# Performance work log

Hardware: AMD Instinct MI355X
Metric: run time of the kernel (lower is better)

Reference implementation:

```python
import jax, jax.numpy as jnp
import numpy as np

N, E, FI, H, T, FO, B = 20000, 320000, 16, 100, 5, 20, 50
EPS = 1e-5


def _glorot(k, shape, fan_in):
    return jax.random.normal(k, shape, jnp.float32) / np.float32(np.sqrt(fan_in))


def setup_inputs():
    key = jax.random.key(0)
    ks = jax.random.split(key, 16)
    inp = {}
    inp['x'] = jax.random.normal(ks[0], (N, FI), jnp.float32)
    inp['edge_index'] = jax.random.randint(ks[1], (2, E), 0, N, jnp.int32)
    inp['edge_attr'] = jax.random.normal(ks[2], (E, 1), jnp.float32)
    inp['batch'] = jnp.sort(jax.random.randint(ks[3], (N,), 0, B, jnp.int32))
    # PNAConv layer 0: input_dim -> hidden (F_in=FI, F_out=FO per tower)
    inp['e0_w'] = _glorot(ks[4], (1, FI), 1); inp['e0_b'] = jnp.zeros((FI,), jnp.float32)
    inp['pre0_w'] = _glorot(ks[5], (T, 3 * FI, FI), 3 * FI); inp['pre0_b'] = jnp.zeros((T, FI), jnp.float32)
    inp['post0_w'] = _glorot(ks[6], (T, 17 * FI, FO), 17 * FI); inp['post0_b'] = jnp.zeros((T, FO), jnp.float32)
    inp['lin0_w'] = _glorot(ks[7], (H, H), H); inp['lin0_b'] = jnp.zeros((H,), jnp.float32)
    inp['bn0_g'] = jnp.ones((H,), jnp.float32); inp['bn0_b'] = jnp.zeros((H,), jnp.float32)
    # PNAConv layers 1..2 (hidden -> hidden), stacked on leading dim 2
    inp['eL_w'] = _glorot(ks[8], (2, 1, H), 1); inp['eL_b'] = jnp.zeros((2, H), jnp.float32)
    inp['preL_w'] = _glorot(ks[9], (2, T, 3 * H, H), 3 * H); inp['preL_b'] = jnp.zeros((2, T, H), jnp.float32)
    inp['postL_w'] = _glorot(ks[10], (2, T, 17 * H, FO), 17 * H); inp['postL_b'] = jnp.zeros((2, T, FO), jnp.float32)
    inp['linL_w'] = _glorot(ks[11], (2, H, H), H); inp['linL_b'] = jnp.zeros((2, H), jnp.float32)
    inp['bnL_g'] = jnp.ones((2, H), jnp.float32); inp['bnL_b'] = jnp.zeros((2, H), jnp.float32)
    # head MLP: H -> 50 -> 25 -> 1
    inp['mlp_w1'] = _glorot(ks[12], (H, 50), H); inp['mlp_b1'] = jnp.zeros((50,), jnp.float32)
    inp['mlp_w2'] = _glorot(ks[13], (50, 25), 50); inp['mlp_b2'] = jnp.zeros((25,), jnp.float32)
    inp['mlp_w3'] = _glorot(ks[14], (25, 1), 25); inp['mlp_b3'] = jnp.zeros((1,), jnp.float32)
    return inp


def _batch_norm(x, g, b):
    mu = x.mean(0)
    var = jnp.mean((x - mu) * (x - mu), 0)  # biased var, as BatchNorm1d (training)
    return (x - mu) * jax.lax.rsqrt(var + EPS) * g + b


def _pna_conv(x, src, dst, edge_attr, cnt, d, log_d, avg_log, avg_lin,
              ew, eb, pw, pb, qw, qb, lw, lb):
    # x: [N,f]; pw: [T,3f,f]; qw: [T,(1+16)f,FO]; lw: [H,H]
    n, f = x.shape
    t = pw.shape[0]
    e = edge_attr @ ew + eb  # [E,f] edge encoder (shared across towers)
    w_i, w_j, w_e = pw[:, :f], pw[:, f:2 * f], pw[:, 2 * f:]
    # pre-MLP on cat([x_i, x_j, e]) without materializing the concat
    m = (jnp.einsum('ef,tfg->etg', x[dst], w_i)
         + jnp.einsum('ef,tfg->etg', x[src], w_j)
         + jnp.einsum('ef,tfg->etg', e, w_e)
         + pb[None])  # [E,T,f]
    dn = d[:, None, None]
    msum = jax.ops.segment_sum(m, dst, n)
    mean = msum / dn
    mean_sq = jax.ops.segment_sum(m * m, dst, n) / dn
    std = jnp.sqrt(jax.nn.relu(mean_sq - mean * mean) + EPS)
    has = (cnt > 0)[:, None, None]
    mn = jnp.where(has, jax.ops.segment_min(m, dst, n), 0.0)
    mx = jnp.where(has, jax.ops.segment_max(m, dst, n), 0.0)
    agg = jnp.concatenate([mean, mn, mx, std], axis=-1)  # [N,T,4f]
    # degree scalers: identity, amplification, attenuation, linear
    scal = jnp.stack([jnp.ones_like(d), log_d / avg_log,
                      avg_log / log_d, d / avg_lin], 0)  # [4,N]
    w_x = qw[:, :f]  # [T,f,FO] block acting on skip features x
    w_s = qw[:, f:].reshape(t, 4, 4 * f, -1).transpose(1, 0, 2, 3)  # [4,T,4f,FO]
    h = (jnp.einsum('nf,tfg->ntg', x, w_x)
         + jnp.einsum('sn,ntf,stfg->ntg', scal, agg, w_s)
         + qb[None])  # [N,T,FO]
    return h.reshape(n, -1) @ lw + lb  # [N,H]


def _model(x, edge_attr, e0_w, e0_b, pre0_w, pre0_b, post0_w, post0_b,
           lin0_w, lin0_b, bn0_g, bn0_b, eL_w, eL_b, preL_w, preL_b,
           postL_w, postL_b, linL_w, linL_b, bnL_g, bnL_b,
           mlp_w1, mlp_b1, mlp_w2, mlp_b2, mlp_w3, mlp_b3,
           edge_index, batch):
    src, dst = edge_index[0], edge_index[1]
    cnt = jax.ops.segment_sum(jnp.ones((E,), x.dtype), dst, N)
    d = jnp.maximum(cnt, 1.0)
    log_d = jnp.log(d + 1.0)
    avg_lin = jnp.mean(cnt)                 # PNA avg_deg['lin']
    avg_log = jnp.mean(jnp.log(cnt + 1.0))  # PNA avg_deg['log']
    h = _pna_conv(x, src, dst, edge_attr, cnt, d, log_d, avg_log, avg_lin,
                  e0_w, e0_b, pre0_w, pre0_b, post0_w, post0_b, lin0_w, lin0_b)
    h = jax.nn.relu(_batch_norm(h, bn0_g, bn0_b))
    for i in range(2):  # zip(convs, batch_norms) -> only num_conv_layers blocks run
        h = _pna_conv(h, src, dst, edge_attr, cnt, d, log_d, avg_log, avg_lin,
                      eL_w[i], eL_b[i], preL_w[i], preL_b[i],
                      postL_w[i], postL_b[i], linL_w[i], linL_b[i])
        h = jax.nn.relu(_batch_norm(h, bnL_g[i], bnL_b[i]))
    # global mean pool over graphs
    gsum = jax.ops.segment_sum(h, batch, B)
    gcnt = jnp.maximum(jax.ops.segment_sum(jnp.ones((N,), h.dtype), batch, B), 1.0)
    g = gsum / gcnt[:, None]
    g = jax.nn.relu(g @ mlp_w1 + mlp_b1)
    g = jax.nn.relu(g @ mlp_w2 + mlp_b2)
    return g @ mlp_w3 + mlp_b3  # [B,1]


def reference(x, edge_attr, e0_w, e0_b, pre0_w, pre0_b, post0_w, post0_b,
              lin0_w, lin0_b, bn0_g, bn0_b, eL_w, eL_b, preL_w, preL_b,
              postL_w, postL_b, linL_w, linL_b, bnL_g, bnL_b,
              mlp_w1, mlp_b1, mlp_w2, mlp_b2, mlp_w3, mlp_b3,
              edge_index, batch):
    return _model(x, edge_attr, e0_w, e0_b, pre0_w, pre0_b, post0_w, post0_b,
                  lin0_w, lin0_b, bn0_g, bn0_b, eL_w, eL_b, preL_w, preL_b,
                  postL_w, postL_b, linL_w, linL_b, bnL_g, bnL_b,
                  mlp_w1, mlp_b1, mlp_w2, mlp_b2, mlp_w3, mlp_b3,
                  edge_index, batch)
```

## Files before the change

kernel.cpp:

```cpp
#include <hip/hip_runtime.h>
#include <hip/hip_bf16.h>
#include <cstddef>

#define N_  20000
#define E_  320000
#define FI_ 16
#define H_  100
#define T_  5
#define FO_ 20
#define B_  50
#define EPSF 1e-5f
#define PR_  200

typedef __attribute__((ext_vector_type(8))) short short8;
typedef __attribute__((ext_vector_type(4))) float f32x4;

static __device__ __forceinline__ unsigned short f2bf(float x) {
  unsigned int u = __builtin_bit_cast(unsigned int, x);
  unsigned int r = (u + 0x7FFFu + ((u >> 16) & 1u)) >> 16;
  return (unsigned short)r;
}
static __device__ __forceinline__ unsigned int packbf(float a, float b) {
  return (unsigned int)f2bf(a) | ((unsigned int)f2bf(b) << 16);
}
static __device__ __forceinline__ float bf2f_lo(unsigned int u) {
  return __builtin_bit_cast(float, (u & 0xFFFFu) << 16);
}
static __device__ __forceinline__ float bf2f_hi(unsigned int u) {
  return __builtin_bit_cast(float, u & 0xFFFF0000u);
}

__global__ void k_count(const int* __restrict__ dst, int* __restrict__ cnt) {
  int e = blockIdx.x * blockDim.x + threadIdx.x;
  if (e < E_) atomicAdd(&cnt[dst[e]], 1);
}

__global__ __launch_bounds__(1024) void k_scan(const int* __restrict__ cnt, int* __restrict__ rowptr) {
  __shared__ int ls[1024];
  const int tid = threadIdx.x;
  const int base = tid * 20;
  int loc[20];
  int lsum = 0;
  #pragma unroll
  for (int i = 0; i < 20; ++i) {
    int idx = base + i;
    int v = (idx < N_) ? cnt[idx] : 0;
    loc[i] = lsum;
    lsum += v;
  }
  ls[tid] = lsum;
  __syncthreads();
  for (int off = 1; off < 1024; off <<= 1) {
    int t = (tid >= off) ? ls[tid - off] : 0;
    __syncthreads();
    ls[tid] += t;
    __syncthreads();
  }
  const int pre = (tid > 0) ? ls[tid - 1] : 0;
  #pragma unroll
  for (int i = 0; i < 20; ++i) {
    int idx = base + i;
    if (idx < N_) rowptr[idx] = pre + loc[i];
  }
  if (tid == 1023) rowptr[N_] = ls[1023];
}

__global__ void k_fill(const int* __restrict__ src, const int* __restrict__ dst,
                       const float* __restrict__ ea, const int* __restrict__ rowptr,
                       int* __restrict__ cursor, int* __restrict__ srcs,
                       float* __restrict__ eav) {
  int e = blockIdx.x * blockDim.x + threadIdx.x;
  if (e < E_) {
    int v = dst[e];
    int p = atomicAdd(&cursor[v], 1);
    int pos = rowptr[v] + p;
    srcs[pos] = src[e];
    eav[pos]  = ea[e];
  }
}

__global__ void k_sumlog(const int* __restrict__ cnt, float* __restrict__ sumlog) {
  int i = blockIdx.x * blockDim.x + threadIdx.x;
  float v = (i < N_) ? logf((float)cnt[i] + 1.0f) : 0.0f;
  #pragma unroll
  for (int off = 32; off > 0; off >>= 1) v += __shfl_down(v, off);
  __shared__ float red[4];
  if ((threadIdx.x & 63) == 0) red[threadIdx.x >> 6] = v;
  __syncthreads();
  if (threadIdx.x == 0) atomicAdd(sumlog, red[0] + red[1] + red[2] + red[3]);
}

__global__ void k_scal(const int* __restrict__ cnt, const float* __restrict__ sumlog,
                       float* __restrict__ scal) {
  int i = blockIdx.x * blockDim.x + threadIdx.x;
  if (i >= N_) return;
  float c  = (float)cnt[i];
  float d  = fmaxf(c, 1.0f);
  float ld = logf(d + 1.0f);
  float avg_log = sumlog[0] * (1.0f / (float)N_);
  float avg_lin = (float)E_ / (float)N_;
  scal[i*4+0] = 1.0f;
  scal[i*4+1] = ld / avg_log;
  scal[i*4+2] = avg_log / ld;
  scal[i*4+3] = d / avg_lin;
}

__global__ void k_edgevec(const float* __restrict__ pw, const float* __restrict__ pb,
                          const float* __restrict__ ew, const float* __restrict__ eb,
                          float* __restrict__ vec_e, float* __restrict__ cst_e, int f, int C) {
  int c = blockIdx.x * blockDim.x + threadIdx.x;
  if (c >= C) return;
  int t = c / f, g = c - t*f;
  const float* wp = pw + (size_t)t*3*f*f + (size_t)2*f*f + g;
  float v = 0.f, s = 0.f;
  for (int ff = 0; ff < f; ++ff) { float wv = wp[(size_t)ff*f]; v += ew[ff]*wv; s += eb[ff]*wv; }
  vec_e[c] = v;
  cst_e[c] = s + pb[c];
}

__global__ void k_pack_preT(const float* __restrict__ pw, unsigned short* __restrict__ Bb,
                            int f, int C, int KPk, int NcPad) {
  int tot = NcPad * KPk;
  int idx = blockIdx.x * blockDim.x + threadIdx.x;
  if (idx >= tot) return;
  int k = idx % KPk, c = idx / KPk;
  float v = 0.f;
  if (c < 2*C && k < f) {
    int half = c / C, cc = c - half*C;
    int t = cc / f, g = cc - t*f;
    v = pw[(size_t)t*3*f*f + (size_t)(half*f + k)*f + g];
  }
  Bb[idx] = f2bf(v);
}

__global__ void k_pack_w2(const float* __restrict__ qw, unsigned short* __restrict__ W2,
                          int f, int KP) {
  int tot = T_ * 80 * KP;
  int idx = blockIdx.x * blockDim.x + threadIdx.x;
  if (idx >= tot) return;
  int k = idx % KP;
  int r = idx / KP;
  int j = r % 80;
  int t = r / 80;
  int s = j / 20, g = j - s*20;
  float v = 0.f;
  if (k < 4*f)                 v = qw[((size_t)t*17*f + f + (size_t)s*4*f + k) * FO_ + g];
  else if (k < 5*f && s == 0)  v = qw[((size_t)t*17*f + (k - 4*f)) * FO_ + g];
  W2[idx] = f2bf(v);
}

__global__ void k_pack_lin(const float* __restrict__ lw, unsigned short* __restrict__ Lb) {
  int idx = blockIdx.x * blockDim.x + threadIdx.x;
  if (idx >= 128*128) return;
  int k = idx & 127, j = idx >> 7;
  float v = (j < H_ && k < H_) ? lw[(size_t)k*H_ + j] : 0.f;
  Lb[idx] = f2bf(v);
}

__global__ __launch_bounds__(256) void k_mmsplit(
    const float* __restrict__ A, const unsigned short* __restrict__ Bb,
    float* __restrict__ XI, unsigned short* __restrict__ XJb,
    int M, int K, int KPk, int split)
{
  const int m0 = blockIdx.x * 128;
  const int bn = blockIdx.y * 128;
  const int Nc = 2 * split;
  const int tid = threadIdx.x;
  const int w = tid >> 6, lane = tid & 63;
  const int rl = lane & 15, kq = lane >> 4;
  __shared__ __align__(16) unsigned short As[128*40];
  __shared__ __align__(16) unsigned short Bs[128*40];
  f32x4 acc[2][8];
  #pragma unroll
  for (int mf = 0; mf < 2; ++mf)
    #pragma unroll
    for (int nf = 0; nf < 8; ++nf) acc[mf][nf] = (f32x4){0.f,0.f,0.f,0.f};

  for (int k0 = 0; k0 < KPk; k0 += 32) {
    __syncthreads();
    #pragma unroll
    for (int p = 0; p < 2; ++p) {
      int idx = tid + p*256;
      int row = idx >> 2, q = idx & 3;
      int gm = m0 + row;
      int gk = k0 + q*8;
      unsigned int d0 = 0, d1 = 0, d2 = 0, d3 = 0;
      if (gm < M) {
        if (gk + 8 <= K) {
          const float4 v0 = *(const float4*)&A[(size_t)gm*K + gk];
          const float4 v1 = *(const float4*)&A[(size_t)gm*K + gk + 4];
          d0 = packbf(v0.x, v0.y); d1 = packbf(v0.z, v0.w);
          d2 = packbf(v1.x, v1.y); d3 = packbf(v1.z, v1.w);
        } else if (gk < K) {
          float tmp[8];
          #pragma unroll
          for (int e = 0; e < 8; ++e) tmp[e] = (gk + e < K) ? A[(size_t)gm*K + gk + e] : 0.f;
          d0 = packbf(tmp[0], tmp[1]); d1 = packbf(tmp[2], tmp[3]);
          d2 = packbf(tmp[4], tmp[5]); d3 = packbf(tmp[6], tmp[7]);
        }
      }
      uint4 dv = {d0, d1, d2, d3};
      *(uint4*)&As[row*40 + q*8] = dv;
    }
    #pragma unroll
    for (int p = 0; p < 2; ++p) {
      int idx = tid + p*256;
      int j = idx >> 2, q = idx & 3;
      uint4 v = *(const uint4*)&Bb[((size_t)(bn + j))*KPk + k0 + q*8];
      *(uint4*)&Bs[j*40 + q*8] = v;
    }
    __syncthreads();
    short8 af[2], bf[8];
    #pragma unroll
    for (int mf = 0; mf < 2; ++mf)
      af[mf] = *(const short8*)&As[(w*32 + mf*16 + rl)*40 + kq*8];
    #pragma unroll
    for (int nf = 0; nf < 8; ++nf)
      bf[nf] = *(const short8*)&Bs[(nf*16 + rl)*40 + kq*8];
    #pragma unroll
    for (int mf = 0; mf < 2; ++mf)
      #pragma unroll
      for (int nf = 0; nf < 8; ++nf)
        acc[mf][nf] = __builtin_amdgcn_mfma_f32_16x16x32_bf16(af[mf], bf[nf], acc[mf][nf], 0, 0, 0);
  }
  #pragma unroll
  for (int mf = 0; mf < 2; ++mf)
    #pragma unroll
    for (int nf = 0; nf < 8; ++nf)
      #pragma unroll
      for (int r = 0; r < 4; ++r) {
        int gm = m0 + w*32 + mf*16 + kq*4 + r;
        int gn = bn + nf*16 + rl;
        if (gm < M && gn < Nc) {
          float v = acc[mf][nf][r];
          if (gn < split) XI[(size_t)gm*split + gn] = v;
          else            XJb[(size_t)gm*split + (gn - split)] = f2bf(v);
        }
      }
}

__global__ __launch_bounds__(256) void k_lin(
    const float* __restrict__ A, const unsigned short* __restrict__ Bb,
    const float* __restrict__ bias, float* __restrict__ Cm, int M)
{
  const int m0 = blockIdx.x * 64;
  const int tid = threadIdx.x;
  const int w = tid >> 6, lane = tid & 63;
  const int rl = lane & 15, kq = lane >> 4;
  __shared__ __align__(16) unsigned short As[64*40];
  __shared__ __align__(16) unsigned short Bs[128*40];
  f32x4 acc[8];
  #pragma unroll
  for (int nf = 0; nf < 8; ++nf) acc[nf] = (f32x4){0.f,0.f,0.f,0.f};
  for (int k0 = 0; k0 < 128; k0 += 32) {
    __syncthreads();
    {
      int row = tid >> 2, q = tid & 3;
      int gm = m0 + row;
      int gk = k0 + q*8;
      unsigned int d0=0,d1=0,d2=0,d3=0;
      if (gm < M && gk < H_) {
        if (gk + 8 <= H_) {
          const float4 v0 = *(const float4*)&A[(size_t)gm*H_ + gk];
          const float4 v1 = *(const float4*)&A[(size_t)gm*H_ + gk + 4];
          d0 = packbf(v0.x,v0.y); d1 = packbf(v0.z,v0.w);
          d2 = packbf(v1.x,v1.y); d3 = packbf(v1.z,v1.w);
        } else {
          float tmp[8];
          #pragma unroll
          for (int e = 0; e < 8; ++e) tmp[e] = (gk+e < H_) ? A[(size_t)gm*H_ + gk + e] : 0.f;
          d0 = packbf(tmp[0],tmp[1]); d1 = packbf(tmp[2],tmp[3]);
          d2 = packbf(tmp[4],tmp[5]); d3 = packbf(tmp[6],tmp[7]);
        }
      }
      uint4 dv = {d0,d1,d2,d3};
      *(uint4*)&As[row*40 + q*8] = dv;
    }
    #pragma unroll
    for (int p = 0; p < 2; ++p) {
      int idx = tid + p*256;
      int j = idx >> 2, q = idx & 3;
      uint4 v = *(const uint4*)&Bb[(size_t)j*128 + k0 + q*8];
      *(uint4*)&Bs[j*40 + q*8] = v;
    }
    __syncthreads();
    short8 af = *(const short8*)&As[(w*16 + rl)*40 + kq*8];
    #pragma unroll
    for (int nf = 0; nf < 8; ++nf) {
      short8 bf = *(const short8*)&Bs[(nf*16 + rl)*40 + kq*8];
      acc[nf] = __builtin_amdgcn_mfma_f32_16x16x32_bf16(af, bf, acc[nf], 0, 0, 0);
    }
  }
  #pragma unroll
  for (int nf = 0; nf < 8; ++nf)
    #pragma unroll
    for (int r = 0; r < 4; ++r) {
      int gm = m0 + w*16 + kq*4 + r;
      int gn = nf*16 + rl;
      if (gm < M && gn < H_)
        Cm[(size_t)gm*H_ + gn] = acc[nf][r] + bias[gn];
    }
}

__global__ __launch_bounds__(256) void k_agg(
    const float* __restrict__ XI, const unsigned short* __restrict__ XJb,
    const int* __restrict__ rowptr, const int* __restrict__ srcs,
    const float* __restrict__ eav, const float* __restrict__ vec_e,
    const float* __restrict__ cst_e, const float* __restrict__ xin,
    unsigned short* __restrict__ Apost, int f, int C, int KP)
{
  __shared__ float vsh[512];
  const int tid = threadIdx.x;
  for (int c = tid; c < C; c += 256) vsh[c] = vec_e[c];
  __syncthreads();
  const int v = blockIdx.x;
  const int start = rowptr[v], end = rowptr[v+1];
  const int half = C >> 1;
  const bool act = (tid < half);
  const float v0 = act ? vsh[tid*2]   : 0.f;
  const float v1 = act ? vsh[tid*2+1] : 0.f;
  const unsigned int* xj = (const unsigned int*)XJb;
  float s10 = 0.f, s11 = 0.f, s20 = 0.f, s21 = 0.f;
  float mn0 = 1e30f, mn1 = 1e30f, mx0 = -1e30f, mx1 = -1e30f;

  int p = start;
  for (; p + 8 <= end; p += 8) {
    int ss[8]; float aa[8];
    #pragma unroll
    for (int q = 0; q < 8; ++q) { ss[q] = srcs[p+q]; aa[q] = eav[p+q]; }
    if (act) {
      unsigned int uu[8];
      #pragma unroll
      for (int q = 0; q < 8; ++q) uu[q] = xj[(size_t)ss[q]*half + tid];
      #pragma unroll
      for (int q = 0; q < 8; ++q) {
        float y0 = fmaf(aa[q], v0, bf2f_lo(uu[q]));
        float y1 = fmaf(aa[q], v1, bf2f_hi(uu[q]));
        s10 += y0; s20 = fmaf(y0,y0,s20); mn0 = fminf(mn0,y0); mx0 = fmaxf(mx0,y0);
        s11 += y1; s21 = fmaf(y1,y1,s21); mn1 = fminf(mn1,y1); mx1 = fmaxf(mx1,y1);
      }
    }
  }
  for (; p < end; ++p) {
    int s = srcs[p];
    float a = eav[p];
    if (act) {
      unsigned int u = xj[(size_t)s*half + tid];
      float y0 = fmaf(a, v0, bf2f_lo(u));
      float y1 = fmaf(a, v1, bf2f_hi(u));
      s10 += y0; s20 = fmaf(y0, y0, s20);
      s11 += y1; s21 = fmaf(y1, y1, s21);
      mn0 = fminf(mn0, y0); mx0 = fmaxf(mx0, y0);
      mn1 = fminf(mn1, y1); mx1 = fmaxf(mx1, y1);
    }
  }

  const int dcnt = end - start;
  if (act) {
    int c0 = tid*2;
    int t = c0 / f, ff = c0 - t*f;
    float base0 = XI[(size_t)v*C + c0]     + cst_e[c0];
    float base1 = XI[(size_t)v*C + c0 + 1] + cst_e[c0 + 1];
    float me0, sd0, lo0, hi0, me1, sd1, lo1, hi1;
    if (dcnt > 0) {
      float inv = 1.0f / (float)dcnt;
      float m10 = s10 * inv, m11 = s11 * inv;
      me0 = base0 + m10; me1 = base1 + m11;
      sd0 = sqrtf(fmaxf(s20*inv - m10*m10, 0.f) + EPSF);
      sd1 = sqrtf(fmaxf(s21*inv - m11*m11, 0.f) + EPSF);
      lo0 = base0 + mn0; hi0 = base0 + mx0;
      lo1 = base1 + mn1; hi1 = base1 + mx1;
    } else {
      me0 = me1 = lo0 = lo1 = hi0 = hi1 = 0.f;
      sd0 = sd1 = sqrtf(EPSF);
    }
    unsigned int* od = (unsigned int*)(Apost + ((size_t)v * T_ + t) * KP);
    int fd = ff >> 1, f2 = f >> 1;
    od[fd]          = packbf(me0, me1);
    od[f2 + fd]     = packbf(lo0, lo1);
    od[2*f2 + fd]   = packbf(hi0, hi1);
    od[3*f2 + fd]   = packbf(sd0, sd1);
  }
  const int rem = KP - 4*f;
  for (int idx = tid; idx < T_*rem; idx += 256) {
    int t = idx / rem, kk = idx - t*rem;
    int k = 4*f + kk;
    unsigned short val = 0;
    if (k < 5*f) val = f2bf(xin[(size_t)v*f + (k - 4*f)]);
    Apost[((size_t)v * T_ + t) * KP + k] = val;
  }
}

__global__ __launch_bounds__(256) void k_postmm(
    const unsigned short* __restrict__ Apost, const unsigned short* __restrict__ W2,
    const float* __restrict__ scal, const float* __restrict__ qb,
    float* __restrict__ h, int KP)
{
  const int t    = blockIdx.y;
  const int m0   = blockIdx.x * 128;
  const int tid  = threadIdx.x;
  const int w    = tid >> 6;
  const int lane = tid & 63;
  const int rl   = lane & 15;
  const int kq   = lane >> 4;
  __shared__ __align__(16) unsigned char smem[128*84*4];
  unsigned short* As = (unsigned short*)smem;
  unsigned short* Bs = As + 128*40;
  f32x4 acc[2][5];
  #pragma unroll
  for (int mf = 0; mf < 2; ++mf)
    #pragma unroll
    for (int nf = 0; nf < 5; ++nf) acc[mf][nf] = (f32x4){0.f,0.f,0.f,0.f};

  const unsigned short* wt = W2 + (size_t)t * 80 * KP;

  for (int k0 = 0; k0 < KP; k0 += 32) {
    __syncthreads();
    #pragma unroll
    for (int p = 0; p < 2; ++p) {
      int idx = tid + p*256;
      int row = idx >> 2, q = idx & 3;
      int gm = m0 + row;
      uint4 v = {0u,0u,0u,0u};
      if (gm < N_) v = *(const uint4*)&Apost[((size_t)gm*T_ + t)*KP + k0 + q*8];
      *(uint4*)&As[row*40 + q*8] = v;
    }
    #pragma unroll
    for (int p = 0; p < 2; ++p) {
      int idx = tid + p*256;
      if (idx < 320) {
        int j = idx >> 2, q = idx & 3;
        uint4 v = *(const uint4*)&wt[(size_t)j*KP + k0 + q*8];
        *(uint4*)&Bs[j*40 + q*8] = v;
      }
    }
    __syncthreads();
    short8 af[2], bf[5];
    #pragma unroll
    for (int mf = 0; mf < 2; ++mf)
      af[mf] = *(const short8*)&As[(w*32 + mf*16 + rl)*40 + kq*8];
    #pragma unroll
    for (int nf = 0; nf < 5; ++nf)
      bf[nf] = *(const short8*)&Bs[(nf*16 + rl)*40 + kq*8];
    #pragma unroll
    for (int mf = 0; mf < 2; ++mf)
      #pragma unroll
      for (int nf = 0; nf < 5; ++nf)
        acc[mf][nf] = __builtin_amdgcn_mfma_f32_16x16x32_bf16(af[mf], bf[nf], acc[mf][nf], 0, 0, 0);
  }
  __syncthreads();
  float (*Pl)[84] = (float (*)[84])smem;
  #pragma unroll
  for (int mf = 0; mf < 2; ++mf)
    #pragma unroll
    for (int nf = 0; nf < 5; ++nf)
      #pragma unroll
      for (int r = 0; r < 4; ++r)
        Pl[w*32 + mf*16 + kq*4 + r][nf*16 + rl] = acc[mf][nf][r];
  __syncthreads();
  for (int idx = tid; idx < 128*FO_; idx += 256) {
    int row = idx / FO_, g = idx - row*FO_;
    int n = m0 + row;
    if (n < N_) {
      const float* p = Pl[row];
      float4 sc = *(const float4*)&scal[n*4];
      h[(size_t)n*(T_*FO_) + t*FO_ + g] =
        p[g] + sc.y*p[20+g] + sc.z*p[40+g] + sc.w*p[60+g] + qb[t*FO_+g];
    }
  }
}

__global__ __launch_bounds__(256) void k_bnsum(const float* __restrict__ h2, float* __restrict__ bnsum) {
  const int tid  = threadIdx.x;
  const int c    = tid & 127;
  const int half = tid >> 7;
  if (c >= H_) return;
  float s = 0.f, s2 = 0.f;
  for (int r = blockIdx.x * 2 + half; r < N_; r += 256) {
    float v = h2[(size_t)r * H_ + c];
    s += v; s2 = fmaf(v, v, s2);
  }
  atomicAdd(&bnsum[c], s);
  atomicAdd(&bnsum[H_ + c], s2);
}

__global__ void k_bnapply(const float* __restrict__ h2, const float* __restrict__ bnsum,
                          const float* __restrict__ gam, const float* __restrict__ bet,
                          float* __restrict__ out) {
  size_t i = (size_t)blockIdx.x * blockDim.x + threadIdx.x;
  if (i >= (size_t)N_*H_) return;
  int c = (int)(i % H_);
  const float invn = 1.0f / (float)N_;
  float mu  = bnsum[c] * invn;
  float var = bnsum[H_ + c] * invn - mu*mu;
  float y = (h2[i] - mu) * rsqrtf(var + EPSF) * gam[c] + bet[c];
  out[i] = fmaxf(y, 0.f);
}

__global__ __launch_bounds__(256) void k_pool(const float* __restrict__ xc, const int* __restrict__ batch,
                                              float* __restrict__ gsum, int* __restrict__ gcnt) {
  __shared__ float Pl[B_][H_];
  __shared__ int cl[B_];
  const int tid = threadIdx.x;
  for (int i = tid; i < B_*H_; i += 256) Pl[i / H_][i % H_] = 0.f;
  for (int i = tid; i < B_; i += 256) cl[i] = 0;
  __syncthreads();
  const int r0 = blockIdx.x * PR_;
  const int rend = (r0 + PR_ < N_) ? r0 + PR_ : N_;
  for (int rr = tid; rr < rend - r0; rr += 256) atomicAdd(&cl[batch[r0 + rr]], 1);
  const int nel = (rend - r0) * H_;
  for (int idx = tid; idx < nel; idx += 256) {
    int rr = idx / H_, c = idx - rr*H_;
    int n = r0 + rr;
    atomicAdd(&Pl[batch[n]][c], xc[(size_t)n*H_ + c]);
  }
  __syncthreads();
  const int blo = batch[r0], bhi = batch[rend-1];
  const int nb = (bhi - blo + 1) * H_;
  for (int idx = tid; idx < nb; idx += 256) {
    int b = blo + idx / H_, c = idx % H_;
    atomicAdd(&gsum[(size_t)b*H_ + c], Pl[b][c]);
  }
  for (int b = blo + tid; b <= bhi; b += 256) atomicAdd(&gcnt[b], cl[b]);
}

__global__ __launch_bounds__(512) void k_mlp(
    const float* __restrict__ gsum, const int* __restrict__ gcnt,
    const float* __restrict__ w1, const float* __restrict__ b1,
    const float* __restrict__ w2, const float* __restrict__ b2,
    const float* __restrict__ w3, const float* __restrict__ b3,
    float* __restrict__ out)
{
  __shared__ float G[B_][H_];
  __shared__ float A1[B_][50];
  __shared__ float A2[B_][25];
  const int tid = threadIdx.x;
  for (int i = tid; i < B_*H_; i += 512) {
    int r = i / H_;
    G[r][i - r*H_] = gsum[i] / fmaxf((float)gcnt[r], 1.0f);
  }
  __syncthreads();
  for (int i = tid; i < B_*50; i += 512) {
    int r = i / 50, c = i - r*50;
    float a = b1[c];
    for (int k = 0; k < H_; ++k) a = fmaf(G[r][k], w1[k*50 + c], a);
    A1[r][c] = fmaxf(a, 0.f);
  }
  __syncthreads();
  for (int i = tid; i < B_*25; i += 512) {
    int r = i / 25, c = i - r*25;
    float a = b2[c];
    for (int k = 0; k < 50; ++k) a = fmaf(A1[r][k], w2[k*25 + c], a);
    A2[r][c] = fmaxf(a, 0.f);
  }
  __syncthreads();
  for (int i = tid; i < B_; i += 512) {
    float a = b3[0];
    for (int k = 0; k < 25; ++k) a = fmaf(A2[i][k], w3[k], a);
    out[i] = a;
  }
}

extern "C" void kernel_launch(void* const* d_in, const int* in_sizes, int n_in,
                              void* d_out, int out_size, void* d_ws, size_t ws_size,
                              hipStream_t stream)
{
  (void)in_sizes; (void)n_in; (void)out_size;
  const float* x0   = (const float*)d_in[0];
  const int*   eidx = (const int*)  d_in[1];
  const float* ea   = (const float*)d_in[2];
  const int*   batch= (const int*)  d_in[3];
  const float* e0w  = (const float*)d_in[4];
  const float* e0b  = (const float*)d_in[5];
  const float* p0w  = (const float*)d_in[6];
  const float* p0b  = (const float*)d_in[7];
  const float* q0w  = (const float*)d_in[8];
  const float* q0b  = (const float*)d_in[9];
  const float* l0w  = (const float*)d_in[10];
  const float* l0b  = (const float*)d_in[11];
  const float* g0   = (const float*)d_in[12];
  const float* b0   = (const float*)d_in[13];
  const float* eLw  = (const float*)d_in[14];
  const float* eLb  = (const float*)d_in[15];
  const float* pLw  = (const float*)d_in[16];
  const float* pLb  = (const float*)d_in[17];
  const float* qLw  = (const float*)d_in[18];
  const float* qLb  = (const float*)d_in[19];
  const float* lLw  = (const float*)d_in[20];
  const float* lLb  = (const float*)d_in[21];
  const float* gL   = (const float*)d_in[22];
  const float* bL   = (const float*)d_in[23];
  const float* w1   = (const float*)d_in[24];
  const float* b1   = (const float*)d_in[25];
  const float* w2   = (const float*)d_in[26];
  const float* b2   = (const float*)d_in[27];
  const float* w3   = (const float*)d_in[28];
  const float* b3   = (const float*)d_in[29];

  const int* src = eidx;
  const int* dst = eidx + E_;

  char* w = (char*)d_ws;
  size_t off = 0;
  auto take = [&](size_t bytes) -> void* {
    void* p = (void*)(w + off);
    off = (off + bytes + 255) & ~(size_t)255;
    return p;
  };
  int*   cnt    = (int*)  take((size_t)N_*4);
  int*   rowptr = (int*)  take((size_t)(N_+1)*4);
  int*   cursor = (int*)  take((size_t)N_*4);
  int*   srcs   = (int*)  take((size_t)E_*4);
  float* eav    = (float*)take((size_t)E_*4);
  float* scal   = (float*)take((size_t)N_*16);
  float* sumlog = (float*)take(256);
  float* bnsum  = (float*)take((size_t)2*H_*4);
  float* vec_e  = (float*)take((size_t)T_*H_*4);
  float* cst_e  = (float*)take((size_t)T_*H_*4);
  unsigned short* BpreT = (unsigned short*)take((size_t)1024*128*2);
  unsigned short* W2 = (unsigned short*)take((size_t)T_*80*512*2);
  unsigned short* LwT = (unsigned short*)take((size_t)128*128*2);
  float* XI     = (float*)take((size_t)N_*T_*H_*4);
  unsigned short* XJb = (unsigned short*)take((size_t)N_*T_*H_*2);
  unsigned short* Apost = (unsigned short*)take((size_t)N_*T_*512*2);
  float* hbuf   = (float*)take((size_t)N_*H_*4);
  float* h2buf  = (float*)take((size_t)N_*H_*4);
  float* xcur   = (float*)take((size_t)N_*H_*4);
  float* gsum   = (float*)take((size_t)B_*H_*4);
  int*   gcnt   = (int*)  take((size_t)B_*4);
  if (off > ws_size) return;

  hipMemsetAsync(cnt,    0, (size_t)N_*4, stream);
  hipMemsetAsync(cursor, 0, (size_t)N_*4, stream);
  hipMemsetAsync(sumlog, 0, 4, stream);
  hipMemsetAsync(gsum,   0, (size_t)B_*H_*4, stream);
  hipMemsetAsync(gcnt,   0, (size_t)B_*4, stream);

  k_count <<<dim3((E_+255)/256), dim3(256), 0, stream>>>(dst, cnt);
  k_scan  <<<dim3(1),            dim3(1024),0, stream>>>(cnt, rowptr);
  k_fill  <<<dim3((E_+255)/256), dim3(256), 0, stream>>>(src, dst, ea, rowptr, cursor, srcs, eav);
  k_sumlog<<<dim3((N_+255)/256), dim3(256), 0, stream>>>(cnt, sumlog);
  k_scal  <<<dim3((N_+255)/256), dim3(256), 0, stream>>>(cnt, sumlog, scal);

  auto layer = [&](const float* xin, int f,
                   const float* ew, const float* eb, const float* pw, const float* pb,
                   const float* qw, const float* qb, const float* lw, const float* lb,
                   const float* bg, const float* bb) {
    const int C   = T_ * f;
    const int KP  = ((5*f + 31) / 32) * 32;
    const int KPk = ((f + 31) / 32) * 32;
    const int gN  = (2*C + 127) / 128;
    const int NcPad = gN * 128;
    k_edgevec<<<dim3((C+255)/256), dim3(256), 0, stream>>>(pw, pb, ew, eb, vec_e, cst_e, f, C);
    const int pt = NcPad * KPk;
    k_pack_preT<<<dim3((pt+255)/256), dim3(256), 0, stream>>>(pw, BpreT, f, C, KPk, NcPad);
    const int wtot = T_ * 80 * KP;
    k_pack_w2<<<dim3((wtot+255)/256), dim3(256), 0, stream>>>(qw, W2, f, KP);
    k_pack_lin<<<dim3((128*128+255)/256), dim3(256), 0, stream>>>(lw, LwT);
    k_mmsplit<<<dim3((N_+127)/128, gN), dim3(256), 0, stream>>>(xin, BpreT, XI, XJb, N_, f, KPk, C);
    k_agg<<<dim3(N_), dim3(256), 0, stream>>>(XI, XJb, rowptr, srcs, eav, vec_e, cst_e, xin, Apost, f, C, KP);
    k_postmm<<<dim3((N_+127)/128, T_), dim3(256), 0, stream>>>(Apost, W2, scal, qb, hbuf, KP);
    k_lin<<<dim3((N_+63)/64), dim3(256), 0, stream>>>(hbuf, LwT, lb, h2buf, N_);
    hipMemsetAsync(bnsum, 0, (size_t)2*H_*4, stream);
    k_bnsum<<<dim3(128), dim3(256), 0, stream>>>(h2buf, bnsum);
    k_bnapply<<<dim3((unsigned)(((size_t)N_*H_+255)/256)), dim3(256), 0, stream>>>(h2buf, bnsum, bg, bb, xcur);
  };

  layer(x0,   FI_, e0w, e0b, p0w, p0b, q0w, q0b, l0w, l0b, g0, b0);
  layer(xcur, H_,  eLw, eLb, pLw, pLb, qLw, qLb, lLw, lLb, gL, bL);
  layer(xcur, H_,  eLw + H_, eLb + H_,
        pLw + (size_t)T_*3*H_*H_, pLb + T_*H_,
        qLw + (size_t)T_*17*H_*FO_, qLb + T_*FO_,
        lLw + H_*H_, lLb + H_, gL + H_, bL + H_);

  k_pool<<<dim3((N_+PR_-1)/PR_), dim3(256), 0, stream>>>(xcur, batch, gsum, gcnt);
  k_mlp <<<dim3(1), dim3(512), 0, stream>>>(gsum, gcnt, w1, b1, w2, b2, w3, b3, (float*)d_out);
}
```

Baseline: 835.1 us.

## Batch weight packing across layers, store XI in bf16, shrink layer-0 agg blocks

```diff
diff --git a/kernel.cpp b/kernel.cpp
--- a/kernel.cpp
+++ b/kernel.cpp
@@ -105,24 +105,39 @@
   scal[i*4+3] = d / avg_lin;
 }
 
-__global__ void k_edgevec(const float* __restrict__ pw, const float* __restrict__ pb,
-                          const float* __restrict__ ew, const float* __restrict__ eb,
-                          float* __restrict__ vec_e, float* __restrict__ cst_e, int f, int C) {
+__global__ void k_edgevec3(const float* __restrict__ p0w, const float* __restrict__ pLw,
+                           const float* __restrict__ p0b, const float* __restrict__ pLb,
+                           const float* __restrict__ e0w, const float* __restrict__ eLw,
+                           const float* __restrict__ e0b, const float* __restrict__ eLb,
+                           float* __restrict__ vec_e3, float* __restrict__ cst_e3) {
+  const int l = blockIdx.y;
+  const int f = l ? H_ : FI_;
+  const int C = T_ * f;
   int c = blockIdx.x * blockDim.x + threadIdx.x;
   if (c >= C) return;
+  const float* pw = l ? pLw + (size_t)(l-1)*T_*3*H_*H_ : p0w;
+  const float* pb = l ? pLb + (l-1)*T_*H_ : p0b;
+  const float* ew = l ? eLw + (l-1)*H_ : e0w;
+  const float* eb = l ? eLb + (l-1)*H_ : e0b;
   int t = c / f, g = c - t*f;
   const float* wp = pw + (size_t)t*3*f*f + (size_t)2*f*f + g;
   float v = 0.f, s = 0.f;
   for (int ff = 0; ff < f; ++ff) { float wv = wp[(size_t)ff*f]; v += ew[ff]*wv; s += eb[ff]*wv; }
-  vec_e[c] = v;
-  cst_e[c] = s + pb[c];
-}
-
-__global__ void k_pack_preT(const float* __restrict__ pw, unsigned short* __restrict__ Bb,
-                            int f, int C, int KPk, int NcPad) {
-  int tot = NcPad * KPk;
+  vec_e3[l*512 + c] = v;
+  cst_e3[l*512 + c] = s + pb[c];
+}
+
+__global__ void k_pack_preT3(const float* __restrict__ p0w, const float* __restrict__ pLw,
+                             unsigned short* __restrict__ Bb3) {
+  const int l = blockIdx.y;
+  const int f = l ? H_ : FI_;
+  const int C = T_ * f;
+  const int KPk = l ? 128 : 32;
+  const int NcPad = l ? 1024 : 256;
+  const int tot = NcPad * KPk;
   int idx = blockIdx.x * blockDim.x + threadIdx.x;
   if (idx >= tot) return;
+  const float* pw = l ? pLw + (size_t)(l-1)*T_*3*H_*H_ : p0w;
   int k = idx % KPk, c = idx / KPk;
   float v = 0.f;
   if (c < 2*C && k < f) {
@@ -130,14 +145,18 @@
     int t = cc / f, g = cc - t*f;
     v = pw[(size_t)t*3*f*f + (size_t)(half*f + k)*f + g];
   }
-  Bb[idx] = f2bf(v);
-}
-
-__global__ void k_pack_w2(const float* __restrict__ qw, unsigned short* __restrict__ W2,
-                          int f, int KP) {
-  int tot = T_ * 80 * KP;
+  Bb3[(size_t)l*131072 + idx] = f2bf(v);
+}
+
+__global__ void k_pack_w23(const float* __restrict__ q0w, const float* __restrict__ qLw,
+                           unsigned short* __restrict__ W23) {
+  const int l = blockIdx.y;
+  const int f = l ? H_ : FI_;
+  const int KP = l ? 512 : 96;
+  const int tot = T_ * 80 * KP;
   int idx = blockIdx.x * blockDim.x + threadIdx.x;
   if (idx >= tot) return;
+  const float* qw = l ? qLw + (size_t)(l-1)*T_*17*H_*FO_ : q0w;
   int k = idx % KP;
   int r = idx / KP;
   int j = r % 80;
@@ -146,20 +165,23 @@
   float v = 0.f;
   if (k < 4*f)                 v = qw[((size_t)t*17*f + f + (size_t)s*4*f + k) * FO_ + g];
   else if (k < 5*f && s == 0)  v = qw[((size_t)t*17*f + (k - 4*f)) * FO_ + g];
-  W2[idx] = f2bf(v);
-}
-
-__global__ void k_pack_lin(const float* __restrict__ lw, unsigned short* __restrict__ Lb) {
+  W23[(size_t)l*204800 + idx] = f2bf(v);
+}
+
+__global__ void k_pack_lin3(const float* __restrict__ l0w, const float* __restrict__ lLw,
+                            unsigned short* __restrict__ Lb3) {
+  const int l = blockIdx.y;
   int idx = blockIdx.x * blockDim.x + threadIdx.x;
   if (idx >= 128*128) return;
+  const float* lw = l ? lLw + (size_t)(l-1)*H_*H_ : l0w;
   int k = idx & 127, j = idx >> 7;
   float v = (j < H_ && k < H_) ? lw[(size_t)k*H_ + j] : 0.f;
-  Lb[idx] = f2bf(v);
+  Lb3[(size_t)l*16384 + idx] = f2bf(v);
 }
 
 __global__ __launch_bounds__(256) void k_mmsplit(
     const float* __restrict__ A, const unsigned short* __restrict__ Bb,
-    float* __restrict__ XI, unsigned short* __restrict__ XJb,
+    unsigned short* __restrict__ XIb, unsigned short* __restrict__ XJb,
     int M, int K, int KPk, int split)
 {
   const int m0 = blockIdx.x * 128;
@@ -232,9 +254,9 @@
         int gm = m0 + w*32 + mf*16 + kq*4 + r;
         int gn = bn + nf*16 + rl;
         if (gm < M && gn < Nc) {
-          float v = acc[mf][nf][r];
-          if (gn < split) XI[(size_t)gm*split + gn] = v;
-          else            XJb[(size_t)gm*split + (gn - split)] = f2bf(v);
+          unsigned short v = f2bf(acc[mf][nf][r]);
+          if (gn < split) XIb[(size_t)gm*split + gn] = v;
+          else            XJb[(size_t)gm*split + (gn - split)] = v;
         }
       }
 }
@@ -302,8 +324,9 @@
     }
 }
 
-__global__ __launch_bounds__(256) void k_agg(
-    const float* __restrict__ XI, const unsigned short* __restrict__ XJb,
+template<int BT>
+__global__ __launch_bounds__(BT) void k_agg(
+    const unsigned short* __restrict__ XIb, const unsigned short* __restrict__ XJb,
     const int* __restrict__ rowptr, const int* __restrict__ srcs,
     const float* __restrict__ eav, const float* __restrict__ vec_e,
     const float* __restrict__ cst_e, const float* __restrict__ xin,
@@ -311,7 +334,7 @@
 {
   __shared__ float vsh[512];
   const int tid = threadIdx.x;
-  for (int c = tid; c < C; c += 256) vsh[c] = vec_e[c];
+  for (int c = tid; c < C; c += BT) vsh[c] = vec_e[c];
   __syncthreads();
   const int v = blockIdx.x;
   const int start = rowptr[v], end = rowptr[v+1];
@@ -359,8 +382,9 @@
   if (act) {
     int c0 = tid*2;
     int t = c0 / f, ff = c0 - t*f;
-    float base0 = XI[(size_t)v*C + c0]     + cst_e[c0];
-    float base1 = XI[(size_t)v*C + c0 + 1] + cst_e[c0 + 1];
+    unsigned int ub = ((const unsigned int*)XIb)[(size_t)v*half + tid];
+    float base0 = bf2f_lo(ub) + cst_e[c0];
+    float base1 = bf2f_hi(ub) + cst_e[c0 + 1];
     float me0, sd0, lo0, hi0, me1, sd1, lo1, hi1;
     if (dcnt > 0) {
       float inv = 1.0f / (float)dcnt;
@@ -382,7 +406,7 @@
     od[3*f2 + fd]   = packbf(sd0, sd1);
   }
   const int rem = KP - 4*f;
-  for (int idx = tid; idx < T_*rem; idx += 256) {
+  for (int idx = tid; idx < T_*rem; idx += BT) {
     int t = idx / rem, kk = idx - t*rem;
     int k = 4*f + kk;
     unsigned short val = 0;
@@ -614,15 +638,15 @@
   float* eav    = (float*)take((size_t)E_*4);
   float* scal   = (float*)take((size_t)N_*16);
   float* sumlog = (float*)take(256);
-  float* bnsum  = (float*)take((size_t)2*H_*4);
-  float* vec_e  = (float*)take((size_t)T_*H_*4);
-  float* cst_e  = (float*)take((size_t)T_*H_*4);
-  unsigned short* BpreT = (unsigned short*)take((size_t)1024*128*2);
-  unsigned short* W2 = (unsigned short*)take((size_t)T_*80*512*2);
-  unsigned short* LwT = (unsigned short*)take((size_t)128*128*2);
-  float* XI     = (float*)take((size_t)N_*T_*H_*4);
-  unsigned short* XJb = (unsigned short*)take((size_t)N_*T_*H_*2);
-  unsigned short* Apost = (unsigned short*)take((size_t)N_*T_*512*2);
+  float* bnsum3 = (float*)take((size_t)3*256*4);
+  float* vec_e3 = (float*)take((size_t)3*512*4);
+  float* cst_e3 = (float*)take((size_t)3*512*4);
+  unsigned short* BpreT3 = (unsigned short*)take((size_t)3*131072*2);
+  unsigned short* W23    = (unsigned short*)take((size_t)3*204800*2);
+  unsigned short* LwT3   = (unsigned short*)take((size_t)3*16384*2);
+  unsigned short* XIb    = (unsigned short*)take((size_t)N_*T_*H_*2);
+  unsigned short* XJb    = (unsigned short*)take((size_t)N_*T_*H_*2);
+  unsigned short* Apost  = (unsigned short*)take((size_t)N_*T_*512*2);
   float* hbuf   = (float*)take((size_t)N_*H_*4);
   float* h2buf  = (float*)take((size_t)N_*H_*4);
   float* xcur   = (float*)take((size_t)N_*H_*4);
@@ -633,8 +657,14 @@
   hipMemsetAsync(cnt,    0, (size_t)N_*4, stream);
   hipMemsetAsync(cursor, 0, (size_t)N_*4, stream);
   hipMemsetAsync(sumlog, 0, 4, stream);
+  hipMemsetAsync(bnsum3, 0, (size_t)3*256*4, stream);
   hipMemsetAsync(gsum,   0, (size_t)B_*H_*4, stream);
   hipMemsetAsync(gcnt,   0, (size_t)B_*4, stream);
+
+  k_edgevec3 <<<dim3(2, 3),   dim3(256), 0, stream>>>(p0w, pLw, p0b, pLb, e0w, eLw, e0b, eLb, vec_e3, cst_e3);
+  k_pack_preT3<<<dim3(512, 3), dim3(256), 0, stream>>>(p0w, pLw, BpreT3);
+  k_pack_w23 <<<dim3(800, 3), dim3(256), 0, stream>>>(q0w, qLw, W23);
+  k_pack_lin3<<<dim3(64, 3),  dim3(256), 0, stream>>>(l0w, lLw, LwT3);
 
   k_count <<<dim3((E_+255)/256), dim3(256), 0, stream>>>(dst, cnt);
   k_scan  <<<dim3(1),            dim3(1024),0, stream>>>(cnt, rowptr);
@@ -642,36 +672,32 @@
   k_sumlog<<<dim3((N_+255)/256), dim3(256), 0, stream>>>(cnt, sumlog);
   k_scal  <<<dim3((N_+255)/256), dim3(256), 0, stream>>>(cnt, sumlog, scal);
 
-  auto layer = [&](const float* xin, int f,
-                   const float* ew, const float* eb, const float* pw, const float* pb,
-                   const float* qw, const float* qb, const float* lw, const float* lb,
-                   const float* bg, const float* bb) {
+  auto layer = [&](int l, const float* xin, int f,
+                   const float* qb, const float* lb, const float* bg, const float* bb) {
     const int C   = T_ * f;
     const int KP  = ((5*f + 31) / 32) * 32;
     const int KPk = ((f + 31) / 32) * 32;
     const int gN  = (2*C + 127) / 128;
-    const int NcPad = gN * 128;
-    k_edgevec<<<dim3((C+255)/256), dim3(256), 0, stream>>>(pw, pb, ew, eb, vec_e, cst_e, f, C);
-    const int pt = NcPad * KPk;
-    k_pack_preT<<<dim3((pt+255)/256), dim3(256), 0, stream>>>(pw, BpreT, f, C, KPk, NcPad);
-    const int wtot = T_ * 80 * KP;
-    k_pack_w2<<<dim3((wtot+255)/256), dim3(256), 0, stream>>>(qw, W2, f, KP);
-    k_pack_lin<<<dim3((128*128+255)/256), dim3(256), 0, stream>>>(lw, LwT);
-    k_mmsplit<<<dim3((N_+127)/128, gN), dim3(256), 0, stream>>>(xin, BpreT, XI, XJb, N_, f, KPk, C);
-    k_agg<<<dim3(N_), dim3(256), 0, stream>>>(XI, XJb, rowptr, srcs, eav, vec_e, cst_e, xin, Apost, f, C, KP);
+    const float* vec_e = vec_e3 + l*512;
+    const float* cst_e = cst_e3 + l*512;
+    const unsigned short* BpreT = BpreT3 + (size_t)l*131072;
+    const unsigned short* W2    = W23    + (size_t)l*204800;
+    const unsigned short* LwT   = LwT3   + (size_t)l*16384;
+    float* bnsum = bnsum3 + l*256;
+    k_mmsplit<<<dim3((N_+127)/128, gN), dim3(256), 0, stream>>>(xin, BpreT, XIb, XJb, N_, f, KPk, C);
+    if (f == FI_)
+      k_agg<64><<<dim3(N_), dim3(64), 0, stream>>>(XIb, XJb, rowptr, srcs, eav, vec_e, cst_e, xin, Apost, f, C, KP);
+    else
+      k_agg<256><<<dim3(N_), dim3(256), 0, stream>>>(XIb, XJb, rowptr, srcs, eav, vec_e, cst_e, xin, Apost, f, C, KP);
     k_postmm<<<dim3((N_+127)/128, T_), dim3(256), 0, stream>>>(Apost, W2, scal, qb, hbuf, KP);
     k_lin<<<dim3((N_+63)/64), dim3(256), 0, stream>>>(hbuf, LwT, lb, h2buf, N_);
-    hipMemsetAsync(bnsum, 0, (size_t)2*H_*4, stream);
     k_bnsum<<<dim3(128), dim3(256), 0, stream>>>(h2buf, bnsum);
     k_bnapply<<<dim3((unsigned)(((size_t)N_*H_+255)/256)), dim3(256), 0, stream>>>(h2buf, bnsum, bg, bb, xcur);
   };
 
-  layer(x0,   FI_, e0w, e0b, p0w, p0b, q0w, q0b, l0w, l0b, g0, b0);
-  layer(xcur, H_,  eLw, eLb, pLw, pLb, qLw, qLb, lLw, lLb, gL, bL);
-  layer(xcur, H_,  eLw + H_, eLb + H_,
-        pLw + (size_t)T_*3*H_*H_, pLb + T_*H_,
-        qLw + (size_t)T_*17*H_*FO_, qLb + T_*FO_,
-        lLw + H_*H_, lLb + H_, gL + H_, bL + H_);
+  layer(0, x0,   FI_, q0b, l0b, g0, b0);
+  layer(1, xcur, H_,  qLb, lLb, gL, bL);
+  layer(2, xcur, H_,  qLb + T_*FO_, lLb + H_, gL + H_, bL + H_);
 
   k_pool<<<dim3((N_+PR_-1)/PR_), dim3(256), 0, stream>>>(xcur, batch, gsum, gcnt);
   k_mlp <<<dim3(1), dim3(512), 0, stream>>>(gsum, gcnt, w1, b1, w2, b2, w3, b3, (float*)d_out);
```

After: 760.3 us. -9.0%, faster.
